# Kernel optimization log

Hardware: AMD Instinct MI355X
Metric: run time of the kernel (lower is better)

The kernel has to match this reference:

```python
import jax, jax.numpy as jnp
import numpy as np

D = 1024
H = 16
DFF = 4096
EPS = 1e-5


def layernorm(x, g, b):
    m = jnp.mean(x, axis=-1, keepdims=True)
    v = jnp.var(x, axis=-1, keepdims=True)
    return (x - m) * jax.lax.rsqrt(v + EPS) * g + b


def setup_inputs() -> dict:
    key = jax.random.key(0)
    ks = jax.random.split(key, 6)
    B, T = 2, 2048
    s = 0.02
    return {
        "x": jax.random.normal(ks[0], (B, T, D), dtype=jnp.float32),
        "W_qkv": jax.random.normal(ks[1], (D, 3 * D), dtype=jnp.float32) * s,
        "W_proj": jax.random.normal(ks[2], (D, D), dtype=jnp.float32) * s,
        "W_fc1": jax.random.normal(ks[3], (D, DFF), dtype=jnp.float32) * s,
        "W_fc2": jax.random.normal(ks[4], (DFF, D), dtype=jnp.float32) * s,
        "ln1_g": jnp.ones((D,), jnp.float32),
        "ln1_b": jnp.zeros((D,), jnp.float32),
        "ln2_g": jnp.ones((D,), jnp.float32),
        "ln2_b": jnp.zeros((D,), jnp.float32),
    }


def reference(x, W_qkv, W_proj, W_fc1, W_fc2, ln1_g, ln1_b, ln2_g, ln2_b):
    B, T, C = x.shape
    hd = C // H

    # --- attention sublayer (pre-norm) ---
    h = layernorm(x, ln1_g, ln1_b)
    qkv = h @ W_qkv                                  # [B,T,3C]
    q, k, v = jnp.split(qkv, 3, axis=-1)
    q = q.reshape(B, T, H, hd).transpose(0, 2, 1, 3)  # [B,H,T,hd]
    k = k.reshape(B, T, H, hd).transpose(0, 2, 1, 3)
    v = v.reshape(B, T, H, hd).transpose(0, 2, 1, 3)
    att = jnp.einsum('bhqd,bhkd->bhqk', q, k) * (1.0 / np.sqrt(hd))
    causal = jnp.tril(jnp.ones((T, T), dtype=bool))
    att = jnp.where(causal, att, jnp.float32(-jnp.inf))
    att = jax.nn.softmax(att, axis=-1)
    y = jnp.einsum('bhqk,bhkd->bhqd', att, v)        # [B,H,T,hd]
    y = y.transpose(0, 2, 1, 3).reshape(B, T, C)
    x = x + y @ W_proj

    # --- MLP sublayer (pre-norm) ---
    h = layernorm(x, ln2_g, ln2_b)
    h = jax.nn.gelu(h @ W_fc1, approximate=False)
    x = x + h @ W_fc2
    return x
```

## Files before the change

kernel.cpp:

```cpp
#include <hip/hip_runtime.h>
#include <hip/hip_bf16.h>
#include <math.h>

typedef __bf16 bf16;
typedef __bf16 bf16x4 __attribute__((ext_vector_type(4)));
typedef __bf16 bf16x8 __attribute__((ext_vector_type(8)));
typedef float f32x4 __attribute__((ext_vector_type(4)));
typedef unsigned int u32;

#define MFMA_BF16(a, b, c) __builtin_amdgcn_mfma_f32_16x16x32_bf16(a, b, c, 0, 0, 0)
#define ASYNC16(g, l)                                                                   \
    __builtin_amdgcn_global_load_lds((const __attribute__((address_space(1))) u32*)(g), \
                                     (__attribute__((address_space(3))) u32*)(l), 16, 0, 0)

__global__ __launch_bounds__(256)
void transpose_cast(const float* __restrict__ in, bf16* __restrict__ out, int rows, int cols) {
    __shared__ float tile[32][33];
    const int tx = threadIdx.x, ty = threadIdx.y;
    const int c0 = blockIdx.x * 32, r0 = blockIdx.y * 32;
    #pragma unroll
    for (int j = 0; j < 4; j++)
        tile[ty + j * 8][tx] = in[(size_t)(r0 + ty + j * 8) * cols + c0 + tx];
    __syncthreads();
    #pragma unroll
    for (int j = 0; j < 4; j++)
        out[(size_t)(c0 + ty + j * 8) * rows + r0 + tx] = (bf16)tile[tx][ty + j * 8];
}

__global__ __launch_bounds__(256)
void transpose_v(const bf16* __restrict__ qkv, bf16* __restrict__ vt) {
    __shared__ bf16 tile[32][33];
    const int tx = threadIdx.x, ty = threadIdx.y;
    const int t0 = blockIdx.x * 32;
    const int d0 = blockIdx.y * 32;
    const int bh = blockIdx.z;
    const int b = bh >> 4, h = bh & 15;
    const bf16* src = qkv + (size_t)b * 2048 * 3072 + 2048 + h * 64;
    #pragma unroll
    for (int j = 0; j < 4; j++)
        tile[ty + j * 8][tx] = src[(size_t)(t0 + ty + j * 8) * 3072 + d0 + tx];
    __syncthreads();
    #pragma unroll
    for (int j = 0; j < 4; j++)
        vt[((size_t)bh * 64 + d0 + ty + j * 8) * 2048 + t0 + tx] = tile[tx][ty + j * 8];
}

__global__ __launch_bounds__(256)
void ln_kernel(const float* __restrict__ x, const float* __restrict__ g,
               const float* __restrict__ bb, bf16* __restrict__ out) {
    const int row = blockIdx.x, tid = threadIdx.x;
    const float4 v = reinterpret_cast<const float4*>(x)[(size_t)row * 256 + tid];
    float s = v.x + v.y + v.z + v.w;
    float sq = v.x * v.x + v.y * v.y + v.z * v.z + v.w * v.w;
    #pragma unroll
    for (int o = 32; o > 0; o >>= 1) { s += __shfl_xor(s, o); sq += __shfl_xor(sq, o); }
    __shared__ float ssum[4], ssq[4];
    const int wave = tid >> 6, lane = tid & 63;
    if (lane == 0) { ssum[wave] = s; ssq[wave] = sq; }
    __syncthreads();
    s = ssum[0] + ssum[1] + ssum[2] + ssum[3];
    sq = ssq[0] + ssq[1] + ssq[2] + ssq[3];
    const float mean = s * (1.0f / 1024.0f);
    const float var = sq * (1.0f / 1024.0f) - mean * mean;
    const float rstd = rsqrtf(var + 1e-5f);
    const float4 gv = reinterpret_cast<const float4*>(g)[tid];
    const float4 bv = reinterpret_cast<const float4*>(bb)[tid];
    bf16x4 o;
    o[0] = (bf16)((v.x - mean) * rstd * gv.x + bv.x);
    o[1] = (bf16)((v.y - mean) * rstd * gv.y + bv.y);
    o[2] = (bf16)((v.z - mean) * rstd * gv.z + bv.z);
    o[3] = (bf16)((v.w - mean) * rstd * gv.w + bv.w);
    reinterpret_cast<bf16x4*>(out)[(size_t)row * 256 + tid] = o;
}

template <int EPI, int BN>
__global__ __launch_bounds__(256)
void gemm_bt(const bf16* __restrict__ A, const bf16* __restrict__ Bt,
             const float* __restrict__ resid, float* __restrict__ outf,
             bf16* __restrict__ outb, int M, int N, int K) {
    constexpr int NB = BN / 32;
    __shared__ bf16 As[128][32];
    __shared__ bf16 Bs[BN][32];
    const int tid = threadIdx.x;
    const int wave = tid >> 6, lane = tid & 63;
    const int lm = lane & 15, lq = lane >> 4;
    const int wm = (wave >> 1) * 64, wn = (wave & 1) * (BN / 2);
    const int bm = blockIdx.y * 128, bn = blockIdx.x * BN;
    const int lr = lane >> 2, lc = (lane & 3) * 8;
    f32x4 acc[4][NB];
    #pragma unroll
    for (int i = 0; i < 4; i++)
        #pragma unroll
        for (int j = 0; j < NB; j++) acc[i][j] = (f32x4){0.f, 0.f, 0.f, 0.f};

    for (int kt = 0; kt < K; kt += 32) {
        ASYNC16(A + (size_t)(bm + wave * 32 + lr) * K + kt + lc, &As[wave * 32][0]);
        ASYNC16(A + (size_t)(bm + wave * 32 + 16 + lr) * K + kt + lc, &As[wave * 32 + 16][0]);
        if (BN == 128) {
            ASYNC16(Bt + (size_t)(bn + wave * 32 + lr) * K + kt + lc, &Bs[wave * 32][0]);
            ASYNC16(Bt + (size_t)(bn + wave * 32 + 16 + lr) * K + kt + lc, &Bs[wave * 32 + 16][0]);
        } else {
            ASYNC16(Bt + (size_t)(bn + wave * 16 + lr) * K + kt + lc, &Bs[wave * 16][0]);
        }
        __syncthreads();
        bf16x8 af[4], bfr[NB];
        #pragma unroll
        for (int i = 0; i < 4; i++) af[i] = *reinterpret_cast<const bf16x8*>(&As[wm + i * 16 + lm][lq * 8]);
        #pragma unroll
        for (int j = 0; j < NB; j++) bfr[j] = *reinterpret_cast<const bf16x8*>(&Bs[wn + j * 16 + lm][lq * 8]);
        #pragma unroll
        for (int i = 0; i < 4; i++)
            #pragma unroll
            for (int j = 0; j < NB; j++)
                acc[i][j] = MFMA_BF16(af[i], bfr[j], acc[i][j]);
        __syncthreads();
    }

    const int r0 = bm + wm, c0 = bn + wn;
    #pragma unroll
    for (int i = 0; i < 4; i++) {
        #pragma unroll
        for (int j = 0; j < NB; j++) {
            #pragma unroll
            for (int e = 0; e < 4; e++) {
                const int row = r0 + i * 16 + lq * 4 + e;
                const int col = c0 + j * 16 + lm;
                const float v = acc[i][j][e];
                const size_t idx = (size_t)row * N + col;
                if (EPI == 0) {
                    outb[idx] = (bf16)v;
                } else if (EPI == 1) {
                    outf[idx] = resid[idx] + v;
                } else {
                    outb[idx] = (bf16)(0.5f * v * (1.0f + erff(v * 0.70710678118654752f)));
                }
            }
        }
    }
}

__global__ __launch_bounds__(256)
void attn_kernel(const bf16* __restrict__ qkv, const bf16* __restrict__ vt,
                 bf16* __restrict__ y) {
    __shared__ bf16 Ks[64][68];
    __shared__ bf16 Vt[64][68];
    __shared__ bf16 Ps[4][16][68];
    const int tid = threadIdx.x, wave = tid >> 6, lane = tid & 63;
    const int lm = lane & 15, lq = lane >> 4;
    const int h = blockIdx.y, b = blockIdx.z;
    const size_t base = (size_t)b * 2048 * 3072;
    const bf16* Kbase = qkv + base + 1024 + h * 64;
    const bf16* Vbase = vt + ((size_t)(b * 16 + h) * 64) * 2048;
    const int skey = tid >> 3, sch = (tid & 7) * 8;
    const float k1 = 0.18033688011112042f;

    bf16x8 ones;
    #pragma unroll
    for (int j = 0; j < 8; j++) ones[j] = (lm == 0) ? (bf16)1.0f : (bf16)0.0f;

    for (int ph = 0; ph < 2; ph++) {
        const int qt = ph ? (int)blockIdx.x : 31 - (int)blockIdx.x;

        const int qrow = qt * 64 + wave * 16 + lm;
        const bf16* qp = qkv + base + (size_t)qrow * 3072 + h * 64 + lq * 8;
        bf16x8 aq0 = *reinterpret_cast<const bf16x8*>(qp);
        bf16x8 aq1 = *reinterpret_cast<const bf16x8*>(qp + 32);
        #pragma unroll
        for (int j = 0; j < 8; j++) {
            aq0[j] = (bf16)((float)aq0[j] * k1);
            aq1[j] = (bf16)((float)aq1[j] * k1);
        }

        f32x4 Oc[4], Ol;
        #pragma unroll
        for (int nt = 0; nt < 4; nt++) Oc[nt] = (f32x4){0.f, 0.f, 0.f, 0.f};
        Ol = (f32x4){0.f, 0.f, 0.f, 0.f};

        bf16x8 pk0, pk1, pv0, pv1;
        {
            const bf16* kp = Kbase + (size_t)skey * 3072 + sch;
            pk0 = *reinterpret_cast<const bf16x8*>(kp);
            pk1 = *reinterpret_cast<const bf16x8*>(kp + (size_t)32 * 3072);
            const bf16* vp = Vbase + (size_t)skey * 2048 + sch;
            pv0 = *reinterpret_cast<const bf16x8*>(vp);
            pv1 = *reinterpret_cast<const bf16x8*>(vp + (size_t)32 * 2048);
        }

        for (int kt2 = 0; kt2 <= qt; kt2++) {
            __syncthreads();
            *reinterpret_cast<bf16x8*>(&Ks[skey][sch])      = pk0;
            *reinterpret_cast<bf16x8*>(&Ks[skey + 32][sch]) = pk1;
            *reinterpret_cast<bf16x8*>(&Vt[skey][sch])      = pv0;
            *reinterpret_cast<bf16x8*>(&Vt[skey + 32][sch]) = pv1;
            __syncthreads();
            if (kt2 < qt) {
                const bf16* kp = Kbase + (size_t)((kt2 + 1) * 64 + skey) * 3072 + sch;
                pk0 = *reinterpret_cast<const bf16x8*>(kp);
                pk1 = *reinterpret_cast<const bf16x8*>(kp + (size_t)32 * 3072);
                const bf16* vp = Vbase + (size_t)skey * 2048 + (kt2 + 1) * 64 + sch;
                pv0 = *reinterpret_cast<const bf16x8*>(vp);
                pv1 = *reinterpret_cast<const bf16x8*>(vp + (size_t)32 * 2048);
            }

            f32x4 Sc[4];
            #pragma unroll
            for (int nt = 0; nt < 4; nt++) Sc[nt] = (f32x4){0.f, 0.f, 0.f, 0.f};
            #pragma unroll
            for (int nt = 0; nt < 4; nt++) {
                const bf16x8 bk0 = *reinterpret_cast<const bf16x8*>(&Ks[nt * 16 + lm][lq * 8]);
                const bf16x8 bk1 = *reinterpret_cast<const bf16x8*>(&Ks[nt * 16 + lm][32 + lq * 8]);
                Sc[nt] = MFMA_BF16(aq0, bk0, Sc[nt]);
                Sc[nt] = MFMA_BF16(aq1, bk1, Sc[nt]);
            }

            const int qb = wave * 16 + lq * 4;
            #pragma unroll
            for (int e = 0; e < 4; e++) {
                #pragma unroll
                for (int nt = 0; nt < 4; nt++) {
                    float sv = Sc[nt][e];
                    if (kt2 == qt && (nt * 16 + lm) > (qb + e)) sv = -1e30f;
                    Ps[wave][lq * 4 + e][nt * 16 + lm] = (bf16)exp2f(sv);
                }
            }

            const bf16x8 ap0 = *reinterpret_cast<const bf16x8*>(&Ps[wave][lm][lq * 8]);
            const bf16x8 ap1 = *reinterpret_cast<const bf16x8*>(&Ps[wave][lm][32 + lq * 8]);
            Ol = MFMA_BF16(ap0, ones, Ol);
            Ol = MFMA_BF16(ap1, ones, Ol);
            #pragma unroll
            for (int nt = 0; nt < 4; nt++) {
                const bf16x8 bv0 = *reinterpret_cast<const bf16x8*>(&Vt[nt * 16 + lm][lq * 8]);
                const bf16x8 bv1 = *reinterpret_cast<const bf16x8*>(&Vt[nt * 16 + lm][32 + lq * 8]);
                Oc[nt] = MFMA_BF16(ap0, bv0, Oc[nt]);
                Oc[nt] = MFMA_BF16(ap1, bv1, Oc[nt]);
            }
        }

        const int qrow0 = qt * 64 + wave * 16 + lq * 4;
        float inv[4];
        #pragma unroll
        for (int e = 0; e < 4; e++) inv[e] = 1.0f / __shfl(Ol[e], lane & 48);
        #pragma unroll
        for (int nt = 0; nt < 4; nt++)
            #pragma unroll
            for (int e = 0; e < 4; e++) {
                const int row = qrow0 + e;
                y[((size_t)b * 2048 + row) * 1024 + h * 64 + nt * 16 + lm] = (bf16)(Oc[nt][e] * inv[e]);
            }
    }
}

extern "C" void kernel_launch(void* const* d_in, const int* in_sizes, int n_in,
                              void* d_out, int out_size, void* d_ws, size_t ws_size,
                              hipStream_t stream) {
    const float* x     = (const float*)d_in[0];
    const float* Wqkv  = (const float*)d_in[1];
    const float* Wproj = (const float*)d_in[2];
    const float* Wfc1  = (const float*)d_in[3];
    const float* Wfc2  = (const float*)d_in[4];
    const float* ln1g  = (const float*)d_in[5];
    const float* ln1b  = (const float*)d_in[6];
    const float* ln2g  = (const float*)d_in[7];
    const float* ln2b  = (const float*)d_in[8];
    float* out = (float*)d_out;
    char* ws = (char*)d_ws;

    bf16*  Wqkvt  = (bf16*)(ws);
    bf16*  Wprojt = (bf16*)(ws + 6291456);
    bf16*  Wfc1t  = (bf16*)(ws + 8388608);
    bf16*  Wfc2t  = (bf16*)(ws + 16777216);
    bf16*  hb     = (bf16*)(ws + 25165824);
    bf16*  vt     = (bf16*)(ws + 25165824);
    bf16*  qkv    = (bf16*)(ws + 33554432);
    bf16*  yb     = (bf16*)(ws + 58720256);
    float* x1     = (float*)(ws + 67108864);
    bf16*  h3     = (bf16*)(ws + 33554432);

    const dim3 tb(32, 8);
    transpose_cast<<<dim3(96, 32), tb, 0, stream>>>(Wqkv, Wqkvt, 1024, 3072);
    transpose_cast<<<dim3(32, 32), tb, 0, stream>>>(Wproj, Wprojt, 1024, 1024);
    transpose_cast<<<dim3(128, 32), tb, 0, stream>>>(Wfc1, Wfc1t, 1024, 4096);
    transpose_cast<<<dim3(32, 128), tb, 0, stream>>>(Wfc2, Wfc2t, 4096, 1024);

    ln_kernel<<<dim3(4096), dim3(256), 0, stream>>>(x, ln1g, ln1b, hb);
    gemm_bt<0, 128><<<dim3(24, 32), dim3(256), 0, stream>>>(hb, Wqkvt, nullptr, nullptr, qkv, 4096, 3072, 1024);
    transpose_v<<<dim3(64, 2, 32), tb, 0, stream>>>(qkv, vt);
    attn_kernel<<<dim3(16, 16, 2), dim3(256), 0, stream>>>(qkv, vt, yb);
    gemm_bt<1, 64><<<dim3(16, 32), dim3(256), 0, stream>>>(yb, Wprojt, x, x1, nullptr, 4096, 1024, 1024);
    ln_kernel<<<dim3(4096), dim3(256), 0, stream>>>(x1, ln2g, ln2b, hb);
    gemm_bt<2, 128><<<dim3(32, 32), dim3(256), 0, stream>>>(hb, Wfc1t, nullptr, nullptr, h3, 4096, 4096, 1024);
    gemm_bt<1, 64><<<dim3(16, 32), dim3(256), 0, stream>>>(h3, Wfc2t, x1, out, nullptr, 4096, 1024, 4096);
}
```

Baseline: 390.9 us.

## Use split-K with atomic accumulation for the projection and FC2 GEMMs

Replaces the residual-epilogue GEMMs (proj and fc2, N=1024) with a split-K kernel. A copy kernel first seeds the output with the residual, then K-slices add their partial sums with float atomicAdd. The intent is more workgroups on the narrow-N GEMMs so the GPU is better occupied (1024 or 2048 blocks instead of 512). The cost is an extra copy pass, atomic traffic on the float output, and a summation order that is no longer deterministic.

```diff
diff --git a/kernel.cpp b/kernel.cpp
--- a/kernel.cpp
+++ b/kernel.cpp
@@ -43,6 +43,15 @@
     #pragma unroll
     for (int j = 0; j < 4; j++)
         vt[((size_t)bh * 64 + d0 + ty + j * 8) * 2048 + t0 + tx] = tile[tx][ty + j * 8];
+}
+
+__global__ __launch_bounds__(256)
+void copy_f32(const float* __restrict__ src, float* __restrict__ dst) {
+    const size_t i = (size_t)blockIdx.x * 512 + threadIdx.x * 2;
+    const float4 a = reinterpret_cast<const float4*>(src)[i];
+    const float4 b = reinterpret_cast<const float4*>(src)[i + 1];
+    reinterpret_cast<float4*>(dst)[i] = a;
+    reinterpret_cast<float4*>(dst)[i + 1] = b;
 }
 
 __global__ __launch_bounds__(256)
@@ -76,7 +85,6 @@
 template <int EPI, int BN>
 __global__ __launch_bounds__(256)
 void gemm_bt(const bf16* __restrict__ A, const bf16* __restrict__ Bt,
-             const float* __restrict__ resid, float* __restrict__ outf,
              bf16* __restrict__ outb, int M, int N, int K) {
     constexpr int NB = BN / 32;
     __shared__ bf16 As[128][32];
@@ -129,14 +137,61 @@
                 const size_t idx = (size_t)row * N + col;
                 if (EPI == 0) {
                     outb[idx] = (bf16)v;
-                } else if (EPI == 1) {
-                    outf[idx] = resid[idx] + v;
                 } else {
                     outb[idx] = (bf16)(0.5f * v * (1.0f + erff(v * 0.70710678118654752f)));
                 }
             }
         }
     }
+}
+
+__global__ __launch_bounds__(256)
+void gemm_bt_splitk(const bf16* __restrict__ A, const bf16* __restrict__ Bt,
+                    float* __restrict__ outf, int M, int N, int K, int Kseg) {
+    __shared__ bf16 As[128][32];
+    __shared__ bf16 Bs[64][32];
+    const int tid = threadIdx.x;
+    const int wave = tid >> 6, lane = tid & 63;
+    const int lm = lane & 15, lq = lane >> 4;
+    const int wm = (wave >> 1) * 64, wn = (wave & 1) * 32;
+    const int bm = blockIdx.y * 128, bn = blockIdx.x * 64;
+    const int k0 = blockIdx.z * Kseg, k1 = k0 + Kseg;
+    const int lr = lane >> 2, lc = (lane & 3) * 8;
+    f32x4 acc[4][2];
+    #pragma unroll
+    for (int i = 0; i < 4; i++)
+        #pragma unroll
+        for (int j = 0; j < 2; j++) acc[i][j] = (f32x4){0.f, 0.f, 0.f, 0.f};
+
+    for (int kt = k0; kt < k1; kt += 32) {
+        ASYNC16(A + (size_t)(bm + wave * 32 + lr) * K + kt + lc, &As[wave * 32][0]);
+        ASYNC16(A + (size_t)(bm + wave * 32 + 16 + lr) * K + kt + lc, &As[wave * 32 + 16][0]);
+        ASYNC16(Bt + (size_t)(bn + wave * 16 + lr) * K + kt + lc, &Bs[wave * 16][0]);
+        __syncthreads();
+        bf16x8 af[4], bfr[2];
+        #pragma unroll
+        for (int i = 0; i < 4; i++) af[i] = *reinterpret_cast<const bf16x8*>(&As[wm + i * 16 + lm][lq * 8]);
+        #pragma unroll
+        for (int j = 0; j < 2; j++) bfr[j] = *reinterpret_cast<const bf16x8*>(&Bs[wn + j * 16 + lm][lq * 8]);
+        #pragma unroll
+        for (int i = 0; i < 4; i++)
+            #pragma unroll
+            for (int j = 0; j < 2; j++)
+                acc[i][j] = MFMA_BF16(af[i], bfr[j], acc[i][j]);
+        __syncthreads();
+    }
+
+    const int r0 = bm + wm, c0 = bn + wn;
+    #pragma unroll
+    for (int i = 0; i < 4; i++)
+        #pragma unroll
+        for (int j = 0; j < 2; j++)
+            #pragma unroll
+            for (int e = 0; e < 4; e++) {
+                const int row = r0 + i * 16 + lq * 4 + e;
+                const int col = c0 + j * 16 + lm;
+                atomicAdd(&outf[(size_t)row * N + col], acc[i][j][e]);
+            }
 }
 
 __global__ __launch_bounds__(256)
@@ -284,11 +339,16 @@
     transpose_cast<<<dim3(32, 128), tb, 0, stream>>>(Wfc2, Wfc2t, 4096, 1024);
 
     ln_kernel<<<dim3(4096), dim3(256), 0, stream>>>(x, ln1g, ln1b, hb);
-    gemm_bt<0, 128><<<dim3(24, 32), dim3(256), 0, stream>>>(hb, Wqkvt, nullptr, nullptr, qkv, 4096, 3072, 1024);
+    gemm_bt<0, 128><<<dim3(24, 32), dim3(256), 0, stream>>>(hb, Wqkvt, qkv, 4096, 3072, 1024);
     transpose_v<<<dim3(64, 2, 32), tb, 0, stream>>>(qkv, vt);
     attn_kernel<<<dim3(16, 16, 2), dim3(256), 0, stream>>>(qkv, vt, yb);
-    gemm_bt<1, 64><<<dim3(16, 32), dim3(256), 0, stream>>>(yb, Wprojt, x, x1, nullptr, 4096, 1024, 1024);
+
+    copy_f32<<<dim3(2048), dim3(256), 0, stream>>>(x, x1);
+    gemm_bt_splitk<<<dim3(16, 32, 2), dim3(256), 0, stream>>>(yb, Wprojt, x1, 4096, 1024, 1024, 512);
+
     ln_kernel<<<dim3(4096), dim3(256), 0, stream>>>(x1, ln2g, ln2b, hb);
-    gemm_bt<2, 128><<<dim3(32, 32), dim3(256), 0, stream>>>(hb, Wfc1t, nullptr, nullptr, h3, 4096, 4096, 1024);
-    gemm_bt<1, 64><<<dim3(16, 32), dim3(256), 0, stream>>>(h3, Wfc2t, x1, out, nullptr, 4096, 1024, 4096);
-}
+    gemm_bt<2, 128><<<dim3(32, 32), dim3(256), 0, stream>>>(hb, Wfc1t, h3, 4096, 4096, 1024);
+
+    copy_f32<<<dim3(2048), dim3(256), 0, stream>>>(x1, out);
+    gemm_bt_splitk<<<dim3(16, 32, 4), dim3(256), 0, stream>>>(h3, Wfc2t, out, 4096, 1024, 4096, 1024);
+}
```

Result: slower. 426.0 us (+9.0%).

## Double GEMM K-tile to 64 with XOR-swizzled LDS layout

Applied to the files above, without the earlier changes.

Raises the GEMM K step from 32 to 64 so each loop iteration loads twice as much data per barrier pair, halving the number of __syncthreads round trips. The global-to-LDS async copies use an XOR swizzle on the 16-byte column chunk, and fragment reads apply the matching inverse swizzle to avoid LDS bank conflicts on the wider rows. This doubles LDS usage per block and raises register pressure from holding two k-slices of fragments, which may reduce occupancy.

```diff
diff --git a/kernel.cpp b/kernel.cpp
--- a/kernel.cpp
+++ b/kernel.cpp
@@ -79,40 +79,56 @@
              const float* __restrict__ resid, float* __restrict__ outf,
              bf16* __restrict__ outb, int M, int N, int K) {
     constexpr int NB = BN / 32;
-    __shared__ bf16 As[128][32];
-    __shared__ bf16 Bs[BN][32];
+    __shared__ bf16 As[128][64];
+    __shared__ bf16 Bs[BN][64];
     const int tid = threadIdx.x;
     const int wave = tid >> 6, lane = tid & 63;
     const int lm = lane & 15, lq = lane >> 4;
     const int wm = (wave >> 1) * 64, wn = (wave & 1) * (BN / 2);
     const int bm = blockIdx.y * 128, bn = blockIdx.x * BN;
-    const int lr = lane >> 2, lc = (lane & 3) * 8;
+    const int lr8 = lane >> 3;
+    const int lg  = ((lane & 7) ^ lr8) * 8;
+    const int sa  = lm & 7;
+    int co[2];
+    co[0] = (lq ^ sa) * 8;
+    co[1] = ((lq ^ 4) ^ sa) * 8;
     f32x4 acc[4][NB];
     #pragma unroll
     for (int i = 0; i < 4; i++)
         #pragma unroll
         for (int j = 0; j < NB; j++) acc[i][j] = (f32x4){0.f, 0.f, 0.f, 0.f};
 
-    for (int kt = 0; kt < K; kt += 32) {
-        ASYNC16(A + (size_t)(bm + wave * 32 + lr) * K + kt + lc, &As[wave * 32][0]);
-        ASYNC16(A + (size_t)(bm + wave * 32 + 16 + lr) * K + kt + lc, &As[wave * 32 + 16][0]);
+    for (int kt = 0; kt < K; kt += 64) {
+        #pragma unroll
+        for (int s = 0; s < 4; s++)
+            ASYNC16(A + (size_t)(bm + wave * 32 + s * 8 + lr8) * K + kt + lg, &As[wave * 32 + s * 8][0]);
         if (BN == 128) {
-            ASYNC16(Bt + (size_t)(bn + wave * 32 + lr) * K + kt + lc, &Bs[wave * 32][0]);
-            ASYNC16(Bt + (size_t)(bn + wave * 32 + 16 + lr) * K + kt + lc, &Bs[wave * 32 + 16][0]);
+            #pragma unroll
+            for (int s = 0; s < 4; s++)
+                ASYNC16(Bt + (size_t)(bn + wave * 32 + s * 8 + lr8) * K + kt + lg, &Bs[wave * 32 + s * 8][0]);
         } else {
-            ASYNC16(Bt + (size_t)(bn + wave * 16 + lr) * K + kt + lc, &Bs[wave * 16][0]);
+            #pragma unroll
+            for (int s = 0; s < 2; s++)
+                ASYNC16(Bt + (size_t)(bn + wave * 16 + s * 8 + lr8) * K + kt + lg, &Bs[wave * 16 + s * 8][0]);
         }
         __syncthreads();
-        bf16x8 af[4], bfr[NB];
-        #pragma unroll
-        for (int i = 0; i < 4; i++) af[i] = *reinterpret_cast<const bf16x8*>(&As[wm + i * 16 + lm][lq * 8]);
-        #pragma unroll
-        for (int j = 0; j < NB; j++) bfr[j] = *reinterpret_cast<const bf16x8*>(&Bs[wn + j * 16 + lm][lq * 8]);
-        #pragma unroll
-        for (int i = 0; i < 4; i++)
+        bf16x8 af[2][4], bfr[2][NB];
+        #pragma unroll
+        for (int kk = 0; kk < 2; kk++) {
+            #pragma unroll
+            for (int i = 0; i < 4; i++)
+                af[kk][i] = *reinterpret_cast<const bf16x8*>(&As[wm + i * 16 + lm][co[kk]]);
             #pragma unroll
             for (int j = 0; j < NB; j++)
-                acc[i][j] = MFMA_BF16(af[i], bfr[j], acc[i][j]);
+                bfr[kk][j] = *reinterpret_cast<const bf16x8*>(&Bs[wn + j * 16 + lm][co[kk]]);
+        }
+        #pragma unroll
+        for (int kk = 0; kk < 2; kk++)
+            #pragma unroll
+            for (int i = 0; i < 4; i++)
+                #pragma unroll
+                for (int j = 0; j < NB; j++)
+                    acc[i][j] = MFMA_BF16(af[kk][i], bfr[kk][j], acc[i][j]);
         __syncthreads();
     }
 
```

After: 364.8 us. -6.7%, faster.

## Double-buffer GEMM LDS tiles, XOR-swizzle LDS layout, use tanh-form GELU

Applied to the files above, without the earlier changes.

The GEMM main loop now uses two LDS buffers, so the next K tile's async global-to-LDS loads are issued while MFMAs run on the current tile. This drops one barrier per iteration. The LDS tile layout is XOR-swizzled on 16-byte groups to reduce bank conflicts on the fragment reads. The erf-based GELU epilogue is replaced with a sigmoid/exp2 form of the tanh approximation, which trades a small numerical deviation for cheaper math. LDS usage doubles, which may reduce occupancy.

```diff
diff --git a/kernel.cpp b/kernel.cpp
--- a/kernel.cpp
+++ b/kernel.cpp
@@ -73,47 +73,64 @@
     reinterpret_cast<bf16x4*>(out)[(size_t)row * 256 + tid] = o;
 }
 
+__device__ __forceinline__ float gelu_fast(float v) {
+    const float vv = v * v;
+    const float u = v * (1.595769122f + 0.0713548162726f * vv);
+    const float t = exp2f(u * -1.4426950408889634f);
+    return v / (1.0f + t);
+}
+
 template <int EPI, int BN>
 __global__ __launch_bounds__(256)
 void gemm_bt(const bf16* __restrict__ A, const bf16* __restrict__ Bt,
              const float* __restrict__ resid, float* __restrict__ outf,
              bf16* __restrict__ outb, int M, int N, int K) {
     constexpr int NB = BN / 32;
-    __shared__ bf16 As[128][32];
-    __shared__ bf16 Bs[BN][32];
+    __shared__ bf16 As[2][128][32];
+    __shared__ bf16 Bs[2][BN][32];
     const int tid = threadIdx.x;
     const int wave = tid >> 6, lane = tid & 63;
     const int lm = lane & 15, lq = lane >> 4;
     const int wm = (wave >> 1) * 64, wn = (wave & 1) * (BN / 2);
     const int bm = blockIdx.y * 128, bn = blockIdx.x * BN;
-    const int lr = lane >> 2, lc = (lane & 3) * 8;
+    const int srow = lane >> 2;
+    const int sg = (((lane & 3) ^ ((lane >> 2) & 3)) * 8);
+    const int pco = (lq ^ (lm & 3)) * 8;
     f32x4 acc[4][NB];
     #pragma unroll
     for (int i = 0; i < 4; i++)
         #pragma unroll
         for (int j = 0; j < NB; j++) acc[i][j] = (f32x4){0.f, 0.f, 0.f, 0.f};
 
+    auto stage = [&](int bb, int kt) {
+        ASYNC16(A + (size_t)(bm + wave * 32 + srow) * K + kt + sg,      &As[bb][wave * 32][0]);
+        ASYNC16(A + (size_t)(bm + wave * 32 + 16 + srow) * K + kt + sg, &As[bb][wave * 32 + 16][0]);
+        if (BN == 128) {
+            ASYNC16(Bt + (size_t)(bn + wave * 32 + srow) * K + kt + sg,      &Bs[bb][wave * 32][0]);
+            ASYNC16(Bt + (size_t)(bn + wave * 32 + 16 + srow) * K + kt + sg, &Bs[bb][wave * 32 + 16][0]);
+        } else {
+            ASYNC16(Bt + (size_t)(bn + wave * 16 + srow) * K + kt + sg,      &Bs[bb][wave * 16][0]);
+        }
+    };
+
+    stage(0, 0);
+    int cur = 0;
     for (int kt = 0; kt < K; kt += 32) {
-        ASYNC16(A + (size_t)(bm + wave * 32 + lr) * K + kt + lc, &As[wave * 32][0]);
-        ASYNC16(A + (size_t)(bm + wave * 32 + 16 + lr) * K + kt + lc, &As[wave * 32 + 16][0]);
-        if (BN == 128) {
-            ASYNC16(Bt + (size_t)(bn + wave * 32 + lr) * K + kt + lc, &Bs[wave * 32][0]);
-            ASYNC16(Bt + (size_t)(bn + wave * 32 + 16 + lr) * K + kt + lc, &Bs[wave * 32 + 16][0]);
-        } else {
-            ASYNC16(Bt + (size_t)(bn + wave * 16 + lr) * K + kt + lc, &Bs[wave * 16][0]);
-        }
         __syncthreads();
+        if (kt + 32 < K) stage(cur ^ 1, kt + 32);
         bf16x8 af[4], bfr[NB];
         #pragma unroll
-        for (int i = 0; i < 4; i++) af[i] = *reinterpret_cast<const bf16x8*>(&As[wm + i * 16 + lm][lq * 8]);
-        #pragma unroll
-        for (int j = 0; j < NB; j++) bfr[j] = *reinterpret_cast<const bf16x8*>(&Bs[wn + j * 16 + lm][lq * 8]);
+        for (int i = 0; i < 4; i++)
+            af[i] = *reinterpret_cast<const bf16x8*>(&As[cur][wm + i * 16 + lm][pco]);
+        #pragma unroll
+        for (int j = 0; j < NB; j++)
+            bfr[j] = *reinterpret_cast<const bf16x8*>(&Bs[cur][wn + j * 16 + lm][pco]);
         #pragma unroll
         for (int i = 0; i < 4; i++)
             #pragma unroll
             for (int j = 0; j < NB; j++)
                 acc[i][j] = MFMA_BF16(af[i], bfr[j], acc[i][j]);
-        __syncthreads();
+        cur ^= 1;
     }
 
     const int r0 = bm + wm, c0 = bn + wn;
@@ -132,7 +149,7 @@
                 } else if (EPI == 1) {
                     outf[idx] = resid[idx] + v;
                 } else {
-                    outb[idx] = (bf16)(0.5f * v * (1.0f + erff(v * 0.70710678118654752f)));
+                    outb[idx] = (bf16)gelu_fast(v);
                 }
             }
         }
```

After: 365.6 us. 1.07x faster.
